# Kernel tuning notes

Hardware: AMD Instinct MI355X
Metric: run time of the kernel (lower is better)

The kernel has to match this reference:

```python
import jax, jax.numpy as jnp
import numpy as np

B_SZ, C_IN, C_OUT, H, W = 16, 32, 32, 128, 128
K, CODE, PAD, FACTOR = 3, 2, 1, 1.0

def setup_inputs() -> dict:
    key = jax.random.key(0)
    ks = jax.random.split(key, 7)
    s = 0.05
    return {
        "x": jax.random.normal(ks[0], (B_SZ, C_IN, H, W), jnp.float32),
        "codes": jax.random.normal(ks[1], (B_SZ, CODE, CODE), jnp.float32),
        "weight": jax.random.normal(ks[2], (C_OUT, C_IN, K, K), jnp.float32) * s,
        "A": jax.random.normal(ks[3], (C_IN, CODE, K, K), jnp.float32) * s,
        "Bm": jax.random.normal(ks[4], (C_OUT, CODE, K, K), jnp.float32) * s,
        "bias": jax.random.normal(ks[5], (C_OUT,), jnp.float32) * s,
        "bias_context": jax.random.normal(ks[6], (CODE, C_OUT), jnp.float32) * s,
    }

def reference(x, codes, weight, A, Bm, bias, bias_context):
    # hypernetwork weight synthesis: [b, out, in, k, k]
    w_ctx = jnp.einsum('ickl,bcr->birkl', A, codes)            # [b, in, code, k, k]
    w_ctx = jnp.einsum('birkl,orkl->boikl', w_ctx, Bm)         # [b, out, in, k, k]
    combined_weight = weight[None] + FACTOR * w_ctx
    # per-sample bias from diagonal of codes
    diag = jnp.diagonal(codes, axis1=-2, axis2=-1)             # [b, code]
    combined_bias = bias[None] + FACTOR * (diag @ bias_context)  # [b, out]
    # circular padding then per-sample VALID conv (== unfold + einsum)
    xp = jnp.pad(x, ((0, 0), (0, 0), (PAD, PAD), (PAD, PAD)), mode='wrap')
    def conv_one(xi, wi):
        return jax.lax.conv_general_dilated(
            xi[None], wi, window_strides=(1, 1), padding='VALID',
            dimension_numbers=('NCHW', 'OIHW', 'NCHW'))[0]
    out = jax.vmap(conv_one)(xp, combined_weight)              # [b, out, H, W]
    return out + combined_bias[:, :, None, None]
```

## Files before the change

### kernel.cpp

```cpp
#include <hip/hip_runtime.h>

typedef short bf16x8 __attribute__((ext_vector_type(8)));
typedef float f32x4  __attribute__((ext_vector_type(4)));
typedef unsigned int u32;

#define HH 128
#define WW 128

__device__ __forceinline__ u32 cvt_pk_bf16(float lo, float hi) {
    u32 r;
    asm volatile("v_cvt_pk_bf16_f32 %0, %1, %2" : "=v"(r) : "v"(lo), "v"(hi));
    return r;
}

__device__ __forceinline__ void lds_barrier() {
    asm volatile("s_waitcnt lgkmcnt(0)" ::: "memory");
    __builtin_amdgcn_s_barrier();
    __builtin_amdgcn_sched_barrier(0);
}

__global__ __launch_bounds__(1024, 1) void geps_mfma_kernel(
    const float* __restrict__ x, const float* __restrict__ codes,
    const float* __restrict__ weight, const float* __restrict__ A,
    const float* __restrict__ Bm, const float* __restrict__ bias,
    const float* __restrict__ bctx, float* __restrict__ out)
{
    __shared__ bf16x8 lds_x[5120];
    __shared__ bf16x8 lds_w[1152];
    __shared__ float  lds_b[32];

    const int tid  = threadIdx.x;
    const int l    = tid & 63;
    const int wvid = tid >> 6;
    const int row4 = wvid >> 2;
    const int nq   = wvid & 3;

    const int orig = blockIdx.x;
    const int vb   = (orig & 7) * 32 + (orig >> 3);
    const int b    = vb >> 4;
    const int grp  = vb & 15;
    const int h0   = grp * 8;

    const float c00 = codes[b * 4 + 0];
    const float c01 = codes[b * 4 + 1];
    const float c10 = codes[b * 4 + 2];
    const float c11 = codes[b * 4 + 3];
    float bv = 0.f, bx0 = 0.f, bx1 = 0.f;
    if (tid < 32) { bv = bias[tid]; bx0 = bctx[tid]; bx1 = bctx[32 + tid]; }

    const int j0 = tid, j1 = tid + 1024;
    const int kl0 = j0 >> 7, o0 = (j0 & 127) >> 2, kb0 = j0 & 3;
    float m0a, m1a, wga[8], a0a[8], a1a[8];
    m0a = Bm[(o0 * 2 + 0) * 9 + kl0];
    m1a = Bm[(o0 * 2 + 1) * 9 + kl0];
    #pragma unroll
    for (int jj = 0; jj < 8; ++jj) {
        int i = kb0 * 8 + jj;
        wga[jj] = weight[(o0 * 32 + i) * 9 + kl0];
        a0a[jj] = A[(i * 2 + 0) * 9 + kl0];
        a1a[jj] = A[(i * 2 + 1) * 9 + kl0];
    }
    const int kl1 = j1 >> 7, o1 = (j1 & 127) >> 2, kb1 = j1 & 3;
    float m0b = 0, m1b = 0, wgb[8], a0b[8], a1b[8];
    if (tid < 128) {
        m0b = Bm[(o1 * 2 + 0) * 9 + kl1];
        m1b = Bm[(o1 * 2 + 1) * 9 + kl1];
        #pragma unroll
        for (int jj = 0; jj < 8; ++jj) {
            int i = kb1 * 8 + jj;
            wgb[jj] = weight[(o1 * 32 + i) * 9 + kl1];
            a0b[jj] = A[(i * 2 + 0) * 9 + kl1];
            a1b[jj] = A[(i * 2 + 1) * 9 + kl1];
        }
    }

    float2 f[3][4];
    #pragma unroll
    for (int it = 0; it < 3; ++it) {
        int idx = it * 1024 + tid;
        int cp = idx & 63, jh = (idx >> 6) & 1, ig = (idx >> 7) & 3, rr = idx >> 9;
        int grow = (h0 - 1 + rr) & 127;
        const float* src =
            x + ((size_t)(b * 32 + ig * 8 + jh * 4) * HH + grow) * WW + cp * 2;
        #pragma unroll
        for (int jj = 0; jj < 4; ++jj)
            f[it][jj] = *(const float2*)(src + (size_t)jj * HH * WW);
    }

    {
        float wf[8];
        #pragma unroll
        for (int jj = 0; jj < 8; ++jj) {
            float t0 = a0a[jj] * c00 + a1a[jj] * c10;
            float t1 = a0a[jj] * c01 + a1a[jj] * c11;
            wf[jj] = wga[jj] + t0 * m0a + t1 * m1a;
        }
        u32 pk[4];
        #pragma unroll
        for (int q = 0; q < 4; ++q) pk[q] = cvt_pk_bf16(wf[2 * q], wf[2 * q + 1]);
        *(uint4*)&lds_w[kl0 * 128 + (o0 >> 4) * 64 + kb0 * 16 + (o0 & 15)] =
            make_uint4(pk[0], pk[1], pk[2], pk[3]);
    }
    if (tid < 128) {
        float wf[8];
        #pragma unroll
        for (int jj = 0; jj < 8; ++jj) {
            float t0 = a0b[jj] * c00 + a1b[jj] * c10;
            float t1 = a0b[jj] * c01 + a1b[jj] * c11;
            wf[jj] = wgb[jj] + t0 * m0b + t1 * m1b;
        }
        u32 pk[4];
        #pragma unroll
        for (int q = 0; q < 4; ++q) pk[q] = cvt_pk_bf16(wf[2 * q], wf[2 * q + 1]);
        *(uint4*)&lds_w[kl1 * 128 + (o1 >> 4) * 64 + kb1 * 16 + (o1 & 15)] =
            make_uint4(pk[0], pk[1], pk[2], pk[3]);
    }
    if (tid < 32) lds_b[tid] = bv + c00 * bx0 + c11 * bx1;

    #pragma unroll
    for (int it = 0; it < 3; ++it) {
        int idx = it * 1024 + tid;
        int cp = idx & 63, jh = (idx >> 6) & 1, ig = (idx >> 7) & 3, rr = idx >> 9;
        int c0 = cp * 2;
        u32 a0 = cvt_pk_bf16(f[it][0].x, f[it][1].x);
        u32 a1 = cvt_pk_bf16(f[it][2].x, f[it][3].x);
        u32 b0 = cvt_pk_bf16(f[it][0].y, f[it][1].y);
        u32 b1 = cvt_pk_bf16(f[it][2].y, f[it][3].y);
        int didx = (c0 >> 4) * 64 + ig * 16 + (c0 & 15);
        *(uint2*)((char*)lds_x + rr * 8192 + didx * 16 + jh * 8) =
            make_uint2(a0, a1);
        *(uint2*)((char*)lds_x + rr * 8192 + (didx + 1) * 16 + jh * 8) =
            make_uint2(b0, b1);
    }

    float2 fd[2][4];
    #pragma unroll
    for (int it = 0; it < 2; ++it) {
        int idx = it * 1024 + tid;
        int cp = idx & 63, jh = (idx >> 6) & 1, ig = (idx >> 7) & 3;
        int rr = 6 + (idx >> 9);
        int grow = (h0 - 1 + rr) & 127;
        const float* src =
            x + ((size_t)(b * 32 + ig * 8 + jh * 4) * HH + grow) * WW + cp * 2;
        #pragma unroll
        for (int jj = 0; jj < 4; ++jj)
            fd[it][jj] = *(const float2*)(src + (size_t)jj * HH * WW);
    }

    lds_barrier();

    const int awb = (l >> 4) * 16 + (l & 15);
    bf16x8 af0[9];
    #pragma unroll
    for (int kl = 0; kl < 9; ++kl)
        af0[kl] = lds_w[kl * 128 + awb];

    const int p = l & 15, igf = l >> 4;
    int bb[3];
    #pragma unroll
    for (int dl = -1; dl <= 1; ++dl) {
        int pq = p + dl;
        bb[dl + 1] = (pq & 15) + ((pq >> 4) << 6) + igf * 16;
    }

    float blr[2][4];
    #pragma unroll
    for (int oh = 0; oh < 2; ++oh)
        #pragma unroll
        for (int r = 0; r < 4; ++r)
            blr[oh][r] = lds_b[oh * 16 + (l >> 4) * 4 + r];

    f32x4 acc[2][2];
    #pragma unroll
    for (int oh = 0; oh < 2; ++oh)
        #pragma unroll
        for (int q = 0; q < 2; ++q) acc[oh][q] = (f32x4){0.f, 0.f, 0.f, 0.f};

    #pragma unroll
    for (int lc = 0; lc < 3; ++lc) {
        #pragma unroll
        for (int k = 0; k < 3; ++k) {
            const bf16x8 a0 = af0[k * 3 + lc];
            const bf16x8 a1 = lds_w[(k * 3 + lc) * 128 + 64 + awb];
            const int s = row4 + k;
            #pragma unroll
            for (int q = 0; q < 2; ++q) {
                int t = (bb[lc] + (nq * 2 + q) * 64) & 511;
                bf16x8 bfv = lds_x[s * 512 + t];
                acc[0][q] = __builtin_amdgcn_mfma_f32_16x16x32_bf16(
                    a0, bfv, acc[0][q], 0, 0, 0);
                acc[1][q] = __builtin_amdgcn_mfma_f32_16x16x32_bf16(
                    a1, bfv, acc[1][q], 0, 0, 0);
            }
        }
    }

    #pragma unroll
    for (int it = 0; it < 2; ++it) {
        int idx = it * 1024 + tid;
        int cp = idx & 63, jh = (idx >> 6) & 1, ig = (idx >> 7) & 3;
        int rr = 6 + (idx >> 9);
        int c0 = cp * 2;
        u32 a0 = cvt_pk_bf16(fd[it][0].x, fd[it][1].x);
        u32 a1 = cvt_pk_bf16(fd[it][2].x, fd[it][3].x);
        u32 b0 = cvt_pk_bf16(fd[it][0].y, fd[it][1].y);
        u32 b1 = cvt_pk_bf16(fd[it][2].y, fd[it][3].y);
        int didx = (c0 >> 4) * 64 + ig * 16 + (c0 & 15);
        *(uint2*)((char*)lds_x + rr * 8192 + didx * 16 + jh * 8) =
            make_uint2(a0, a1);
        *(uint2*)((char*)lds_x + rr * 8192 + (didx + 1) * 16 + jh * 8) =
            make_uint2(b0, b1);
    }

    {
        float* bounce = (float*)lds_x;
        #pragma unroll
        for (int oh = 0; oh < 2; ++oh) {
            lds_barrier();
            #pragma unroll
            for (int q = 0; q < 2; ++q)
                #pragma unroll
                for (int r = 0; r < 4; ++r) {
                    int o16  = (l >> 4) * 4 + r;
                    int col  = (nq * 2 + q) * 16 + (l & 15);
                    int col2 = (col + o16 * 4) & 127;
                    bounce[(o16 * 4 + row4) * 128 + col2] =
                        acc[oh][q][r] + blr[oh][r];
                }
            lds_barrier();
            const int ch = oh * 16 + wvid;
            #pragma unroll
            for (int k2 = 0; k2 < 2; ++k2) {
                int hrow = 2 * k2 + (l >> 5);
                int lcol = (l & 31) * 4;
                int pcol = (lcol + wvid * 4) & 127;
                f32x4 v = *(const f32x4*)&bounce[(wvid * 4 + hrow) * 128 + pcol];
                __builtin_nontemporal_store(
                    v, (f32x4*)&out[((size_t)(b * 32 + ch) * HH + (h0 + hrow)) *
                                    WW + lcol]);
            }
        }
    }

    #pragma unroll
    for (int oh = 0; oh < 2; ++oh)
        #pragma unroll
        for (int q = 0; q < 2; ++q) acc[oh][q] = (f32x4){0.f, 0.f, 0.f, 0.f};

    #pragma unroll
    for (int lc = 0; lc < 3; ++lc) {
        #pragma unroll
        for (int k = 0; k < 3; ++k) {
            const bf16x8 a0 = af0[k * 3 + lc];
            const bf16x8 a1 = lds_w[(k * 3 + lc) * 128 + 64 + awb];
            const int s = 4 + row4 + k;
            #pragma unroll
            for (int q = 0; q < 2; ++q) {
                int t = (bb[lc] + (nq * 2 + q) * 64) & 511;
                bf16x8 bfv = lds_x[s * 512 + t];
                acc[0][q] = __builtin_amdgcn_mfma_f32_16x16x32_bf16(
                    a0, bfv, acc[0][q], 0, 0, 0);
                acc[1][q] = __builtin_amdgcn_mfma_f32_16x16x32_bf16(
                    a1, bfv, acc[1][q], 0, 0, 0);
            }
        }
    }

    {
        float* bounce = (float*)((char*)lds_x + 4 * 8192);
        #pragma unroll
        for (int oh = 0; oh < 2; ++oh) {
            lds_barrier();
            #pragma unroll
            for (int q = 0; q < 2; ++q)
                #pragma unroll
                for (int r = 0; r < 4; ++r) {
                    int o16  = (l >> 4) * 4 + r;
                    int col  = (nq * 2 + q) * 16 + (l & 15);
                    int col2 = (col + o16 * 4) & 127;
                    bounce[(o16 * 4 + row4) * 128 + col2] =
                        acc[oh][q][r] + blr[oh][r];
                }
            lds_barrier();
            const int ch = oh * 16 + wvid;
            #pragma unroll
            for (int k2 = 0; k2 < 2; ++k2) {
                int hrow = 2 * k2 + (l >> 5);
                int lcol = (l & 31) * 4;
                int pcol = (lcol + wvid * 4) & 127;
                f32x4 v = *(const f32x4*)&bounce[(wvid * 4 + hrow) * 128 + pcol];
                __builtin_nontemporal_store(
                    v, (f32x4*)&out[((size_t)(b * 32 + ch) * HH +
                                     (h0 + 4 + hrow)) * WW + lcol]);
            }
        }
    }
}

extern "C" void kernel_launch(void* const* d_in, const int* in_sizes, int n_in,
                              void* d_out, int out_size, void* d_ws, size_t ws_size,
                              hipStream_t stream) {
    const float* x      = (const float*)d_in[0];
    const float* codes  = (const float*)d_in[1];
    const float* weight = (const float*)d_in[2];
    const float* A      = (const float*)d_in[3];
    const float* Bm     = (const float*)d_in[4];
    const float* bias   = (const float*)d_in[5];
    const float* bctx   = (const float*)d_in[6];
    float* out = (float*)d_out;

    hipLaunchKernelGGL(geps_mfma_kernel, dim3(256), dim3(1024), 0, stream,
                       x, codes, weight, A, Bm, bias, bctx, out);
}
```

Measured before the change: 23.55 us.

## Hoist all x loads first, precompute code-mixed A in LDS, cache both weight halves

All global loads of x (including the deferred rows) are now issued at kernel start, ahead of the weight synthesis, so their latency overlaps the hypernetwork weight computation. The A·codes contraction is computed once per (in, code, tap) into a new LDS table instead of being recomputed per output element, at the cost of an extra barrier. Both output-half weight fragments are kept in registers rather than re-read from LDS inside the MFMA loops, which raises register pressure and holds more loads in flight.

```diff
diff --git a/kernel.cpp b/kernel.cpp
--- a/kernel.cpp
+++ b/kernel.cpp
@@ -27,6 +27,7 @@
 {
     __shared__ bf16x8 lds_x[5120];
     __shared__ bf16x8 lds_w[1152];
+    __shared__ float  lds_ctx[576];
     __shared__ float  lds_b[32];
 
     const int tid  = threadIdx.x;
@@ -41,81 +42,64 @@
     const int grp  = vb & 15;
     const int h0   = grp * 8;
 
+    float2 f[3][4];
+    float2 fd[2][4];
+    #pragma unroll
+    for (int it = 0; it < 3; ++it) {
+        int idx = it * 1024 + tid;
+        int cp = idx & 63, jh = (idx >> 6) & 1, ig = (idx >> 7) & 3, rr = idx >> 9;
+        int grow = (h0 - 1 + rr) & 127;
+        const float* src =
+            x + ((size_t)(b * 32 + ig * 8 + jh * 4) * HH + grow) * WW + cp * 2;
+        #pragma unroll
+        for (int jj = 0; jj < 4; ++jj)
+            f[it][jj] = *(const float2*)(src + (size_t)jj * HH * WW);
+    }
+    #pragma unroll
+    for (int it = 0; it < 2; ++it) {
+        int idx = it * 1024 + tid;
+        int cp = idx & 63, jh = (idx >> 6) & 1, ig = (idx >> 7) & 3;
+        int rr = 6 + (idx >> 9);
+        int grow = (h0 - 1 + rr) & 127;
+        const float* src =
+            x + ((size_t)(b * 32 + ig * 8 + jh * 4) * HH + grow) * WW + cp * 2;
+        #pragma unroll
+        for (int jj = 0; jj < 4; ++jj)
+            fd[it][jj] = *(const float2*)(src + (size_t)jj * HH * WW);
+    }
+
     const float c00 = codes[b * 4 + 0];
     const float c01 = codes[b * 4 + 1];
     const float c10 = codes[b * 4 + 2];
     const float c11 = codes[b * 4 + 3];
-    float bv = 0.f, bx0 = 0.f, bx1 = 0.f;
-    if (tid < 32) { bv = bias[tid]; bx0 = bctx[tid]; bx1 = bctx[32 + tid]; }
-
-    const int j0 = tid, j1 = tid + 1024;
-    const int kl0 = j0 >> 7, o0 = (j0 & 127) >> 2, kb0 = j0 & 3;
-    float m0a, m1a, wga[8], a0a[8], a1a[8];
-    m0a = Bm[(o0 * 2 + 0) * 9 + kl0];
-    m1a = Bm[(o0 * 2 + 1) * 9 + kl0];
-    #pragma unroll
-    for (int jj = 0; jj < 8; ++jj) {
-        int i = kb0 * 8 + jj;
-        wga[jj] = weight[(o0 * 32 + i) * 9 + kl0];
-        a0a[jj] = A[(i * 2 + 0) * 9 + kl0];
-        a1a[jj] = A[(i * 2 + 1) * 9 + kl0];
-    }
-    const int kl1 = j1 >> 7, o1 = (j1 & 127) >> 2, kb1 = j1 & 3;
-    float m0b = 0, m1b = 0, wgb[8], a0b[8], a1b[8];
-    if (tid < 128) {
-        m0b = Bm[(o1 * 2 + 0) * 9 + kl1];
-        m1b = Bm[(o1 * 2 + 1) * 9 + kl1];
+    if (tid < 576) {
+        int j = tid;
+        int i = j / 18, rem = j % 18, r = rem / 9, kl = rem % 9;
+        float a0 = A[(i * 2 + 0) * 9 + kl];
+        float a1 = A[(i * 2 + 1) * 9 + kl];
+        lds_ctx[j] = (r == 0) ? (a0 * c00 + a1 * c10) : (a0 * c01 + a1 * c11);
+    }
+    if (tid < 32) lds_b[tid] = bias[tid] + c00 * bctx[tid] + c11 * bctx[32 + tid];
+    lds_barrier();
+
+    for (int j = tid; j < 1152; j += 1024) {
+        int kl = j >> 7, rem = j & 127, o = rem >> 2, kb = rem & 3;
+        float m0 = Bm[(o * 2 + 0) * 9 + kl];
+        float m1 = Bm[(o * 2 + 1) * 9 + kl];
+        float wf[8];
         #pragma unroll
         for (int jj = 0; jj < 8; ++jj) {
-            int i = kb1 * 8 + jj;
-            wgb[jj] = weight[(o1 * 32 + i) * 9 + kl1];
-            a0b[jj] = A[(i * 2 + 0) * 9 + kl1];
-            a1b[jj] = A[(i * 2 + 1) * 9 + kl1];
-        }
-    }
-
-    float2 f[3][4];
-    #pragma unroll
-    for (int it = 0; it < 3; ++it) {
-        int idx = it * 1024 + tid;
-        int cp = idx & 63, jh = (idx >> 6) & 1, ig = (idx >> 7) & 3, rr = idx >> 9;
-        int grow = (h0 - 1 + rr) & 127;
-        const float* src =
-            x + ((size_t)(b * 32 + ig * 8 + jh * 4) * HH + grow) * WW + cp * 2;
-        #pragma unroll
-        for (int jj = 0; jj < 4; ++jj)
-            f[it][jj] = *(const float2*)(src + (size_t)jj * HH * WW);
-    }
-
-    {
-        float wf[8];
-        #pragma unroll
-        for (int jj = 0; jj < 8; ++jj) {
-            float t0 = a0a[jj] * c00 + a1a[jj] * c10;
-            float t1 = a0a[jj] * c01 + a1a[jj] * c11;
-            wf[jj] = wga[jj] + t0 * m0a + t1 * m1a;
+            int i = kb * 8 + jj;
+            wf[jj] = weight[(o * 32 + i) * 9 + kl]
+                   + lds_ctx[i * 18 + kl] * m0
+                   + lds_ctx[i * 18 + 9 + kl] * m1;
         }
         u32 pk[4];
         #pragma unroll
         for (int q = 0; q < 4; ++q) pk[q] = cvt_pk_bf16(wf[2 * q], wf[2 * q + 1]);
-        *(uint4*)&lds_w[kl0 * 128 + (o0 >> 4) * 64 + kb0 * 16 + (o0 & 15)] =
+        *(uint4*)&lds_w[kl * 128 + (o >> 4) * 64 + kb * 16 + (o & 15)] =
             make_uint4(pk[0], pk[1], pk[2], pk[3]);
     }
-    if (tid < 128) {
-        float wf[8];
-        #pragma unroll
-        for (int jj = 0; jj < 8; ++jj) {
-            float t0 = a0b[jj] * c00 + a1b[jj] * c10;
-            float t1 = a0b[jj] * c01 + a1b[jj] * c11;
-            wf[jj] = wgb[jj] + t0 * m0b + t1 * m1b;
-        }
-        u32 pk[4];
-        #pragma unroll
-        for (int q = 0; q < 4; ++q) pk[q] = cvt_pk_bf16(wf[2 * q], wf[2 * q + 1]);
-        *(uint4*)&lds_w[kl1 * 128 + (o1 >> 4) * 64 + kb1 * 16 + (o1 & 15)] =
-            make_uint4(pk[0], pk[1], pk[2], pk[3]);
-    }
-    if (tid < 32) lds_b[tid] = bv + c00 * bx0 + c11 * bx1;
 
     #pragma unroll
     for (int it = 0; it < 3; ++it) {
@@ -132,28 +116,15 @@
         *(uint2*)((char*)lds_x + rr * 8192 + (didx + 1) * 16 + jh * 8) =
             make_uint2(b0, b1);
     }
-
-    float2 fd[2][4];
-    #pragma unroll
-    for (int it = 0; it < 2; ++it) {
-        int idx = it * 1024 + tid;
-        int cp = idx & 63, jh = (idx >> 6) & 1, ig = (idx >> 7) & 3;
-        int rr = 6 + (idx >> 9);
-        int grow = (h0 - 1 + rr) & 127;
-        const float* src =
-            x + ((size_t)(b * 32 + ig * 8 + jh * 4) * HH + grow) * WW + cp * 2;
-        #pragma unroll
-        for (int jj = 0; jj < 4; ++jj)
-            fd[it][jj] = *(const float2*)(src + (size_t)jj * HH * WW);
-    }
-
     lds_barrier();
 
     const int awb = (l >> 4) * 16 + (l & 15);
-    bf16x8 af0[9];
+    bf16x8 af[9][2];
     #pragma unroll
     for (int kl = 0; kl < 9; ++kl)
-        af0[kl] = lds_w[kl * 128 + awb];
+        #pragma unroll
+        for (int oh = 0; oh < 2; ++oh)
+            af[kl][oh] = lds_w[kl * 128 + oh * 64 + awb];
 
     const int p = l & 15, igf = l >> 4;
     int bb[3];
@@ -180,8 +151,8 @@
     for (int lc = 0; lc < 3; ++lc) {
         #pragma unroll
         for (int k = 0; k < 3; ++k) {
-            const bf16x8 a0 = af0[k * 3 + lc];
-            const bf16x8 a1 = lds_w[(k * 3 + lc) * 128 + 64 + awb];
+            const bf16x8 a0 = af[k * 3 + lc][0];
+            const bf16x8 a1 = af[k * 3 + lc][1];
             const int s = row4 + k;
             #pragma unroll
             for (int q = 0; q < 2; ++q) {
@@ -251,8 +222,8 @@
     for (int lc = 0; lc < 3; ++lc) {
         #pragma unroll
         for (int k = 0; k < 3; ++k) {
-            const bf16x8 a0 = af0[k * 3 + lc];
-            const bf16x8 a1 = lds_w[(k * 3 + lc) * 128 + 64 + awb];
+            const bf16x8 a0 = af[k * 3 + lc][0];
+            const bf16x8 a1 = af[k * 3 + lc][1];
             const int s = 4 + row4 + k;
             #pragma unroll
             for (int q = 0; q < 2; ++q) {
```

After: 24.90 us. 1.06x slower.
